# Performance work log

Measured on AMD Instinct MI355X. Metric: run time of the kernel, lower is better.

The kernel has to match this reference:

```python
import jax, jax.numpy as jnp
import numpy as np

B, L, E, H = 2, 2048, 1024, 16
D = E // H

def setup_inputs() -> dict:
    key = jax.random.key(0)
    ks = jax.random.split(key, 6)
    s = 1.0 / np.sqrt(E)
    return {
        "x": jax.random.normal(ks[0], (B, L, E), dtype=jnp.float32),
        "attention_mask": jnp.ones((B, L), dtype=jnp.float32),
        "Wq": jax.random.normal(ks[1], (E, E), dtype=jnp.float32) * s,
        "Wk": jax.random.normal(ks[2], (E, E), dtype=jnp.float32) * s,
        "Wv": jax.random.normal(ks[3], (E, E), dtype=jnp.float32) * s,
        "Wo": jax.random.normal(ks[4], (E, E), dtype=jnp.float32) * s,
        "bo": jnp.zeros((E,), dtype=jnp.float32),
    }

def reference(x, attention_mask, Wq, Wk, Wv, Wo, bo):
    b, l, e = x.shape
    h, d = H, D

    def proj(W):
        # (B,L,E) @ (E,E)^T -> (B,L,E) -> (B,H,L,D)
        return (x @ W.T).reshape(b, l, h, d).transpose(0, 2, 1, 3)

    q, k, v = proj(Wq), proj(Wk), proj(Wv)

    # multiplicative attention mask on q, k, v (mask shape (B,L) -> (B,1,L,1))
    m = attention_mask[:, None, :, None].astype(x.dtype)
    q, k, v = q * m, k * m, v * m

    scale = 1.0 / np.sqrt(d)
    scores = jnp.einsum('bhqd,bhkd->bhqk', q, k) * scale  # (B,H,L,L)
    causal = jnp.tril(jnp.ones((l, l), dtype=bool))
    scores = jnp.where(causal[None, None], scores, -jnp.inf)
    attn = jax.nn.softmax(scores, axis=-1)
    y = jnp.einsum('bhqk,bhkd->bhqd', attn, v)  # (B,H,L,D)
    y = y.transpose(0, 2, 1, 3).reshape(b, l, e)
    return y @ Wo.T + bo
```

## Files before the change

### kernel.cpp

```cpp
#include <hip/hip_runtime.h>
#include <cstdint>
#include <cstddef>
#include <math.h>

#define BB 2
#define LL 2048
#define EE 1024
#define HH 16
#define DD 64
#define MM (BB*LL)

typedef short short8 __attribute__((ext_vector_type(8)));
typedef float f32x4 __attribute__((ext_vector_type(4)));
typedef float f32x16 __attribute__((ext_vector_type(16)));

#define GPTR __attribute__((address_space(1)))
#define LPTR __attribute__((address_space(3)))

__device__ __forceinline__ unsigned short f32_bf16(float f) {
  union { float f; unsigned u; } c; c.f = f;
  c.u += 0x7fffu + ((c.u >> 16) & 1u);
  return (unsigned short)(c.u >> 16);
}

__device__ __forceinline__ unsigned pk_bf16(float lo, float hi) {
  unsigned r;
  asm("v_cvt_pk_bf16_f32 %0, %1, %2" : "=v"(r) : "v"(lo), "v"(hi));
  return r;
}
__device__ __forceinline__ void swap32(unsigned &a, unsigned &b) {
  asm("v_permlane32_swap_b32 %0, %1" : "+v"(a), "+v"(b));
}
__device__ __forceinline__ float xh_max(float v) {
  union { float f; unsigned u; } a, b;
  a.f = v;
  asm("v_mov_b32 %0, %1" : "=&v"(b.u) : "v"(a.u));
  asm("v_permlane32_swap_b32 %0, %1" : "+v"(a.u), "+v"(b.u));
  return fmaxf(a.f, b.f);
}
__device__ __forceinline__ float xh_sum(float v) {
  union { float f; unsigned u; } a, b;
  a.f = v;
  asm("v_mov_b32 %0, %1" : "=&v"(b.u) : "v"(a.u));
  asm("v_permlane32_swap_b32 %0, %1" : "+v"(a.u), "+v"(b.u));
  return a.f + b.f;
}
__device__ __forceinline__ f32x16 zero16() {
  f32x16 v;
  #pragma unroll
  for (int e = 0; e < 16; ++e) v[e] = 0.f;
  return v;
}

__global__ void cvt_all(const float* __restrict__ x,  const float* __restrict__ wq,
                        const float* __restrict__ wk, const float* __restrict__ wv,
                        const float* __restrict__ wo,
                        unsigned short* __restrict__ xb,  unsigned short* __restrict__ wqb,
                        unsigned short* __restrict__ wkb, unsigned short* __restrict__ wvb,
                        unsigned short* __restrict__ wob)
{
  int i = (blockIdx.x * 256 + threadIdx.x) * 4;
  if (i >= MM * EE + 4 * EE * EE) return;
  const float* s; unsigned short* d; int off;
  if (i < MM * EE) { s = x; d = xb; off = i; }
  else {
    int k = i - MM * EE;
    int w = k >> 20;
    off = k & (EE * EE - 1);
    s = (w == 0) ? wq : (w == 1) ? wk : (w == 2) ? wv : wo;
    d = (w == 0) ? wqb : (w == 1) ? wkb : (w == 2) ? wvb : wob;
  }
  float4 v = *(const float4*)(s + off);
  union { unsigned short s[4]; uint2 u; } o;
  o.s[0] = f32_bf16(v.x); o.s[1] = f32_bf16(v.y);
  o.s[2] = f32_bf16(v.z); o.s[3] = f32_bf16(v.w);
  *(uint2*)(d + off) = o.u;
}

template<int MODE>
__global__ __launch_bounds__(256, 2)
void gemm128(const unsigned short* __restrict__ A,
             const unsigned short* __restrict__ W0,
             const unsigned short* __restrict__ W1,
             const unsigned short* __restrict__ W2,
             const float* __restrict__ mask,
             const float* __restrict__ bias,
             unsigned short* __restrict__ O0,
             unsigned short* __restrict__ O1,
             unsigned short* __restrict__ O2,
             float* __restrict__ OF)
{
  constexpr int K = EE;
  const int tid = threadIdx.x;
  const int lane = tid & 63;
  const int wid = tid >> 6;
  const int g = lane >> 4, li = lane & 15;
  const int m0 = blockIdx.y * 128;
  const int n0 = blockIdx.x * 128;
  const int z = blockIdx.z;

  const unsigned short* Wp = W0;
  if (MODE == 0) Wp = (z == 0) ? W0 : ((z == 1) ? W1 : W2);

  __shared__ unsigned short As[128 * 64];
  __shared__ unsigned short Bs[128 * 64];

  f32x4 acc[4][4];
  f32x4 zero = {0.f, 0.f, 0.f, 0.f};
  #pragma unroll
  for (int i = 0; i < 4; ++i)
    #pragma unroll
    for (int j = 0; j < 4; ++j) acc[i][j] = zero;

  const int wm = (wid >> 1) * 64;
  const int wn = (wid & 1) * 64;

  for (int kt = 0; kt < K; kt += 64) {
    #pragma unroll
    for (int j = 0; j < 4; ++j) {
      int c = j * 256 + tid;
      int row = c >> 3;
      int lcol = ((c & 7) * 16) ^ ((row & 7) << 4);
      __builtin_amdgcn_global_load_lds(
        (const GPTR void*)((const char*)(A + (size_t)(m0 + row) * K + kt) + lcol),
        (LPTR void*)((char*)As + c * 16), 16, 0, 0);
      __builtin_amdgcn_global_load_lds(
        (const GPTR void*)((const char*)(Wp + (size_t)(n0 + row) * K + kt) + lcol),
        (LPTR void*)((char*)Bs + c * 16), 16, 0, 0);
    }
    __syncthreads();

    #pragma unroll
    for (int kk = 0; kk < 2; ++kk) {
      short8 a[4], b[4];
      const int colb = (kk * 32 + g * 8) * 2;
      #pragma unroll
      for (int i = 0; i < 4; ++i) {
        int ar = wm + i * 16 + li;
        a[i] = *(const short8*)((const char*)As + ar * 128 + (colb ^ ((ar & 7) << 4)));
        int br = wn + i * 16 + li;
        b[i] = *(const short8*)((const char*)Bs + br * 128 + (colb ^ ((br & 7) << 4)));
      }
      #pragma unroll
      for (int i = 0; i < 4; ++i)
        #pragma unroll
        for (int j = 0; j < 4; ++j)
          acc[i][j] = __builtin_amdgcn_mfma_f32_16x16x32_bf16(a[i], b[j], acc[i][j], 0, 0, 0);
    }
    __syncthreads();
  }

  if (MODE == 0) {
    if (z == 2) {
      #pragma unroll
      for (int i = 0; i < 4; ++i) {
        int mbase = m0 + wm + i * 16 + g * 4;
        int bb2 = mbase >> 11;
        int l0  = mbase & (LL - 1);
        float mk[4];
        #pragma unroll
        for (int r = 0; r < 4; ++r) mk[r] = mask[mbase + r];
        #pragma unroll
        for (int j = 0; j < 4; ++j) {
          int n = n0 + wn + j * 16 + li;
          int h2 = n >> 6, dd2 = n & 63;
          union { unsigned short s[4]; uint2 u; } o;
          #pragma unroll
          for (int r = 0; r < 4; ++r) o.s[r] = f32_bf16(acc[i][j][r] * mk[r]);
          size_t off = (size_t)(bb2 * HH + h2) * (LL * DD)
                     + (size_t)(l0 >> 5) * (DD * 32) + dd2 * 32 + (l0 & 31);
          *(uint2*)(O2 + off) = o.u;
        }
      }
    } else {
      unsigned short* Op = (z == 0) ? O0 : O1;
      const float sc = (z == 0) ? 0.125f * 1.44269504088896f : 1.0f;
      #pragma unroll
      for (int i = 0; i < 4; ++i) {
        #pragma unroll
        for (int r = 0; r < 4; ++r) {
          int m = m0 + wm + i * 16 + g * 4 + r;
          float mk = mask[m] * sc;
          int bb = m >> 11;
          int l  = m & (LL - 1);
          #pragma unroll
          for (int j = 0; j < 4; ++j) {
            int n = n0 + wn + j * 16 + li;
            int h = n >> 6, d = n & 63;
            size_t off = (((size_t)(bb * HH + h)) * LL + l) * DD + d;
            Op[off] = f32_bf16(acc[i][j][r] * mk);
          }
        }
      }
    }
  } else {
    #pragma unroll
    for (int i = 0; i < 4; ++i) {
      #pragma unroll
      for (int j = 0; j < 4; ++j) {
        int n = n0 + wn + j * 16 + li;
        float bv = bias[n];
        #pragma unroll
        for (int r = 0; r < 4; ++r) {
          int m = m0 + wm + i * 16 + g * 4 + r;
          OF[(size_t)m * EE + n] = acc[i][j][r] + bv;
        }
      }
    }
  }
}

__global__ __launch_bounds__(128)
void attn4(const unsigned short* __restrict__ Q,
           const unsigned short* __restrict__ K,
           const unsigned short* __restrict__ VT,
           unsigned short* __restrict__ Y)
{
  const int tid = threadIdx.x, lane = tid & 63, w = tid >> 6;
  const int l31 = lane & 31, hi = lane >> 5;

  const int id = blockIdx.x;
  const int lo = id & 7;
  const int r_ = id >> 3;
  const int bh = (r_ & 3) * 8 + lo;
  const int qt = 63 - (r_ >> 2);
  const int q0 = qt * 32;
  const int b = bh >> 4, h = bh & (HH - 1);
  const size_t kbase = (size_t)bh * LL * DD;

  const unsigned short* Kg  = K + kbase;
  const unsigned short* VTg = VT + kbase;

  const int qrow = q0 + l31;
  const int nt = qt + 1;

  short8 qf[4];
  {
    const unsigned short* Qr = Q + kbase + (size_t)qrow * DD + hi * 8;
    #pragma unroll
    for (int kc = 0; kc < 4; ++kc) qf[kc] = *(const short8*)(Qr + kc * 16);
  }

  f32x16 ot0 = zero16(), ot1 = zero16();
  float m = -INFINITY, lsum = 0.f;

  short8 kA[4], vA[4], kB[4], vB[4];

  auto loadtile = [&](short8 (&kk)[4], short8 (&vv)[4], int t2) {
    const int kv0 = t2 << 5;
    const unsigned short* Kp = Kg + ((size_t)(kv0 + l31) << 6) + hi * 8;
    #pragma unroll
    for (int kc = 0; kc < 4; ++kc) kk[kc] = *(const short8*)(Kp + kc * 16);
    const unsigned short* Vp = VTg + (size_t)(kv0 >> 5) * (DD * 32) + l31 * 32 + hi * 8;
    vv[0] = *(const short8*)(Vp);
    vv[1] = *(const short8*)(Vp + 16);
    vv[2] = *(const short8*)(Vp + 32 * 32);
    vv[3] = *(const short8*)(Vp + 32 * 32 + 16);
  };

  loadtile(kA, vA, w);

  auto body = [&](short8 (&ck)[4], short8 (&cv)[4],
                  short8 (&nk)[4], short8 (&nv)[4], int t) {
    if (t + 2 < nt) loadtile(nk, nv, t + 2);

    const int kv0 = t << 5;

    f32x16 s = zero16();
    __builtin_amdgcn_s_setprio(1);
    #pragma unroll
    for (int kc = 0; kc < 4; ++kc)
      s = __builtin_amdgcn_mfma_f32_32x32x16_bf16(ck[kc], qf[kc], s, 0, 0, 0);
    __builtin_amdgcn_s_setprio(0);

    if (t == nt - 1) {
      #pragma unroll
      for (int i = 0; i < 16; ++i) {
        int kvr = (i & 3) + 8 * (i >> 2) + 4 * hi;
        if (kvr > l31) s[i] = -INFINITY;
      }
    }

    float red[8];
    #pragma unroll
    for (int e = 0; e < 8; ++e) red[e] = fmaxf(s[e], s[e + 8]);
    #pragma unroll
    for (int st = 4; st >= 1; st >>= 1)
      #pragma unroll
      for (int e = 0; e < 4; ++e) if (e < st) red[e] = fmaxf(red[e], red[e + st]);
    float mv = xh_max(red[0]);

    if (!__all(mv <= m + 8.0f)) {
      float mnew = fmaxf(m, mv);
      float al = exp2f(m - mnew);
      m = mnew;
      lsum *= al;
      #pragma unroll
      for (int e = 0; e < 16; ++e) { ot0[e] *= al; ot1[e] *= al; }
    }

    float ra[8];
    #pragma unroll
    for (int e = 0; e < 16; ++e) s[e] = exp2f(s[e] - m);
    #pragma unroll
    for (int e = 0; e < 8; ++e) ra[e] = s[e] + s[e + 8];
    #pragma unroll
    for (int st = 4; st >= 1; st >>= 1)
      #pragma unroll
      for (int e = 0; e < 4; ++e) if (e < st) ra[e] += ra[e + st];
    lsum += xh_sum(ra[0]);

    auto mkfrag = [&](int base) -> short8 {
      unsigned a0 = pk_bf16(s[base + 0], s[base + 1]);
      unsigned a1 = pk_bf16(s[base + 2], s[base + 3]);
      unsigned b0 = pk_bf16(s[base + 4], s[base + 5]);
      unsigned b1 = pk_bf16(s[base + 6], s[base + 7]);
      swap32(a0, b0);
      swap32(a1, b1);
      union { unsigned u[4]; short8 s8; } f;
      f.u[0] = a0; f.u[1] = a1; f.u[2] = b0; f.u[3] = b1;
      return f.s8;
    };
    short8 pf0 = mkfrag(0), pf1 = mkfrag(8);

    __builtin_amdgcn_s_setprio(1);
    ot0 = __builtin_amdgcn_mfma_f32_32x32x16_bf16(cv[0], pf0, ot0, 0, 0, 0);
    ot0 = __builtin_amdgcn_mfma_f32_32x32x16_bf16(cv[1], pf1, ot0, 0, 0, 0);
    ot1 = __builtin_amdgcn_mfma_f32_32x32x16_bf16(cv[2], pf0, ot1, 0, 0, 0);
    ot1 = __builtin_amdgcn_mfma_f32_32x32x16_bf16(cv[3], pf1, ot1, 0, 0, 0);
    __builtin_amdgcn_s_setprio(0);
  };

  for (int t = w; t < nt; t += 4) {
    body(kA, vA, kB, vB, t);
    if (t + 2 < nt) body(kB, vB, kA, vA, t + 2);
  }

  __shared__ float mg[64][34];
  if (w == 1) {
    mg[lane][0] = m; mg[lane][1] = lsum;
    #pragma unroll
    for (int e = 0; e < 16; ++e) { mg[lane][2 + e] = ot0[e]; mg[lane][18 + e] = ot1[e]; }
  }
  __syncthreads();
  if (w == 0) {
    float m1 = mg[lane][0], l1 = mg[lane][1];
    float M = fmaxf(m, m1);
    float a0 = exp2f(m - M), a1 = exp2f(m1 - M);
    float Lt = lsum * a0 + l1 * a1;
    float inv = 1.0f / Lt;
    unsigned short* Yr = Y + ((size_t)b * LL + qrow) * EE + h * DD;
    #pragma unroll
    for (int rg = 0; rg < 4; ++rg) {
      union { unsigned short s[4]; uint2 u; } o0, o1;
      #pragma unroll
      for (int e = 0; e < 4; ++e) {
        int i = rg * 4 + e;
        o0.s[e] = f32_bf16((ot0[i] * a0 + mg[lane][2 + i]  * a1) * inv);
        o1.s[e] = f32_bf16((ot1[i] * a0 + mg[lane][18 + i] * a1) * inv);
      }
      *(uint2*)(Yr + rg * 8 + hi * 4) = o0.u;
      *(uint2*)(Yr + 32 + rg * 8 + hi * 4) = o1.u;
    }
  }
}

extern "C" void kernel_launch(void* const* d_in, const int* in_sizes, int n_in,
                              void* d_out, int out_size, void* d_ws, size_t ws_size,
                              hipStream_t stream) {
  const float* x    = (const float*)d_in[0];
  const float* mask = (const float*)d_in[1];
  const float* Wq   = (const float*)d_in[2];
  const float* Wk   = (const float*)d_in[3];
  const float* Wv   = (const float*)d_in[4];
  const float* Wo   = (const float*)d_in[5];
  const float* bo   = (const float*)d_in[6];
  float* out = (float*)d_out;

  char* ws = (char*)d_ws;
  unsigned short* xb  = (unsigned short*)(ws);
  unsigned short* wqb = (unsigned short*)(ws + ((size_t)8  << 20));
  unsigned short* wkb = (unsigned short*)(ws + ((size_t)10 << 20));
  unsigned short* wvb = (unsigned short*)(ws + ((size_t)12 << 20));
  unsigned short* wob = (unsigned short*)(ws + ((size_t)14 << 20));
  unsigned short* Qb  = (unsigned short*)(ws + ((size_t)16 << 20));
  unsigned short* Kb  = (unsigned short*)(ws + ((size_t)24 << 20));
  unsigned short* VTb = (unsigned short*)(ws + ((size_t)32 << 20));
  unsigned short* Yb  = (unsigned short*)(ws + ((size_t)40 << 20));

  cvt_all<<<8192, 256, 0, stream>>>(x, Wq, Wk, Wv, Wo, xb, wqb, wkb, wvb, wob);

  gemm128<0><<<dim3(EE / 128, MM / 128, 3), 256, 0, stream>>>(
      xb, wqb, wkb, wvb, mask, nullptr, Qb, Kb, VTb, nullptr);

  attn4<<<dim3(2048), 128, 0, stream>>>(Qb, Kb, VTb, Yb);

  gemm128<1><<<dim3(EE / 128, MM / 128, 1), 256, 0, stream>>>(
      Yb, wob, nullptr, nullptr, nullptr, bo, nullptr, nullptr, nullptr, out);
}
```

Measured before the change: 121.4 us.

## Pair high and low causal query tiles per block to share K/V loads

Each attention block now handles two query tiles, a late one (63-p) and an early one (p), instead of a single tile. Every block then does roughly the same causal work, and each K/V tile loaded for the long tile is reused for the short tile's QK and PV MFMAs. The grid is halved and the launch bounds gain a min-blocks hint of 2. The cost is roughly double the live registers (two Q fragment sets and two output accumulators) plus a larger LDS merge buffer, which risks spills or lower occupancy.

```diff
diff --git a/kernel.cpp b/kernel.cpp
--- a/kernel.cpp
+++ b/kernel.cpp
@@ -210,8 +210,8 @@
   }
 }
 
-__global__ __launch_bounds__(128)
-void attn4(const unsigned short* __restrict__ Q,
+__global__ __launch_bounds__(128, 2)
+void attn5(const unsigned short* __restrict__ Q,
            const unsigned short* __restrict__ K,
            const unsigned short* __restrict__ VT,
            unsigned short* __restrict__ Y)
@@ -223,26 +223,30 @@
   const int lo = id & 7;
   const int r_ = id >> 3;
   const int bh = (r_ & 3) * 8 + lo;
-  const int qt = 63 - (r_ >> 2);
-  const int q0 = qt * 32;
+  const int p  = r_ >> 2;
+  const int qth = 63 - p;
+  const int qtl = p;
   const int b = bh >> 4, h = bh & (HH - 1);
   const size_t kbase = (size_t)bh * LL * DD;
 
   const unsigned short* Kg  = K + kbase;
   const unsigned short* VTg = VT + kbase;
 
-  const int qrow = q0 + l31;
-  const int nt = qt + 1;
-
-  short8 qf[4];
+  const int qrh = qth * 32 + l31;
+  const int qrl = qtl * 32 + l31;
+
+  short8 qfh[4], qfl[4];
   {
-    const unsigned short* Qr = Q + kbase + (size_t)qrow * DD + hi * 8;
-    #pragma unroll
-    for (int kc = 0; kc < 4; ++kc) qf[kc] = *(const short8*)(Qr + kc * 16);
-  }
-
-  f32x16 ot0 = zero16(), ot1 = zero16();
-  float m = -INFINITY, lsum = 0.f;
+    const unsigned short* Qr = Q + kbase + (size_t)qrh * DD + hi * 8;
+    #pragma unroll
+    for (int kc = 0; kc < 4; ++kc) qfh[kc] = *(const short8*)(Qr + kc * 16);
+    const unsigned short* Qs = Q + kbase + (size_t)qrl * DD + hi * 8;
+    #pragma unroll
+    for (int kc = 0; kc < 4; ++kc) qfl[kc] = *(const short8*)(Qs + kc * 16);
+  }
+
+  f32x16 oh0 = zero16(), oh1 = zero16(), ol0 = zero16(), ol1 = zero16();
+  float mh = -INFINITY, lsh = 0.f, ml = -INFINITY, lsl = 0.f;
 
   short8 kA[4], vA[4], kB[4], vB[4];
 
@@ -260,27 +264,18 @@
 
   loadtile(kA, vA, w);
 
-  auto body = [&](short8 (&ck)[4], short8 (&cv)[4],
-                  short8 (&nk)[4], short8 (&nv)[4], int t) {
-    if (t + 2 < nt) loadtile(nk, nv, t + 2);
-
-    const int kv0 = t << 5;
-
+  auto qk = [&](const short8 (&ck)[4], const short8 (&qf)[4]) -> f32x16 {
     f32x16 s = zero16();
     __builtin_amdgcn_s_setprio(1);
     #pragma unroll
     for (int kc = 0; kc < 4; ++kc)
       s = __builtin_amdgcn_mfma_f32_32x32x16_bf16(ck[kc], qf[kc], s, 0, 0, 0);
     __builtin_amdgcn_s_setprio(0);
-
-    if (t == nt - 1) {
-      #pragma unroll
-      for (int i = 0; i < 16; ++i) {
-        int kvr = (i & 3) + 8 * (i >> 2) + 4 * hi;
-        if (kvr > l31) s[i] = -INFINITY;
-      }
-    }
-
+    return s;
+  };
+
+  auto process = [&](f32x16 s, const short8 (&cv)[4],
+                     float &mq, float &lq, f32x16 &o0, f32x16 &o1) {
     float red[8];
     #pragma unroll
     for (int e = 0; e < 8; ++e) red[e] = fmaxf(s[e], s[e + 8]);
@@ -290,25 +285,25 @@
       for (int e = 0; e < 4; ++e) if (e < st) red[e] = fmaxf(red[e], red[e + st]);
     float mv = xh_max(red[0]);
 
-    if (!__all(mv <= m + 8.0f)) {
-      float mnew = fmaxf(m, mv);
-      float al = exp2f(m - mnew);
-      m = mnew;
-      lsum *= al;
-      #pragma unroll
-      for (int e = 0; e < 16; ++e) { ot0[e] *= al; ot1[e] *= al; }
+    if (!__all(mv <= mq + 8.0f)) {
+      float mnew = fmaxf(mq, mv);
+      float al = exp2f(mq - mnew);
+      mq = mnew;
+      lq *= al;
+      #pragma unroll
+      for (int e = 0; e < 16; ++e) { o0[e] *= al; o1[e] *= al; }
     }
 
     float ra[8];
     #pragma unroll
-    for (int e = 0; e < 16; ++e) s[e] = exp2f(s[e] - m);
+    for (int e = 0; e < 16; ++e) s[e] = exp2f(s[e] - mq);
     #pragma unroll
     for (int e = 0; e < 8; ++e) ra[e] = s[e] + s[e + 8];
     #pragma unroll
     for (int st = 4; st >= 1; st >>= 1)
       #pragma unroll
       for (int e = 0; e < 4; ++e) if (e < st) ra[e] += ra[e + st];
-    lsum += xh_sum(ra[0]);
+    lq += xh_sum(ra[0]);
 
     auto mkfrag = [&](int base) -> short8 {
       unsigned a0 = pk_bf16(s[base + 0], s[base + 1]);
@@ -324,43 +319,83 @@
     short8 pf0 = mkfrag(0), pf1 = mkfrag(8);
 
     __builtin_amdgcn_s_setprio(1);
-    ot0 = __builtin_amdgcn_mfma_f32_32x32x16_bf16(cv[0], pf0, ot0, 0, 0, 0);
-    ot0 = __builtin_amdgcn_mfma_f32_32x32x16_bf16(cv[1], pf1, ot0, 0, 0, 0);
-    ot1 = __builtin_amdgcn_mfma_f32_32x32x16_bf16(cv[2], pf0, ot1, 0, 0, 0);
-    ot1 = __builtin_amdgcn_mfma_f32_32x32x16_bf16(cv[3], pf1, ot1, 0, 0, 0);
+    o0 = __builtin_amdgcn_mfma_f32_32x32x16_bf16(cv[0], pf0, o0, 0, 0, 0);
+    o0 = __builtin_amdgcn_mfma_f32_32x32x16_bf16(cv[1], pf1, o0, 0, 0, 0);
+    o1 = __builtin_amdgcn_mfma_f32_32x32x16_bf16(cv[2], pf0, o1, 0, 0, 0);
+    o1 = __builtin_amdgcn_mfma_f32_32x32x16_bf16(cv[3], pf1, o1, 0, 0, 0);
     __builtin_amdgcn_s_setprio(0);
   };
 
-  for (int t = w; t < nt; t += 4) {
+  auto body = [&](short8 (&ck)[4], short8 (&cv)[4],
+                  short8 (&nk)[4], short8 (&nv)[4], int t) {
+    if (t + 2 <= qth) loadtile(nk, nv, t + 2);
+
+    {
+      f32x16 s = qk(ck, qfh);
+      if (t == qth) {
+        #pragma unroll
+        for (int i = 0; i < 16; ++i) {
+          int kvr = (i & 3) + 8 * (i >> 2) + 4 * hi;
+          if (kvr > l31) s[i] = -INFINITY;
+        }
+      }
+      process(s, cv, mh, lsh, oh0, oh1);
+    }
+    if (t <= qtl) {
+      f32x16 s = qk(ck, qfl);
+      if (t == qtl) {
+        #pragma unroll
+        for (int i = 0; i < 16; ++i) {
+          int kvr = (i & 3) + 8 * (i >> 2) + 4 * hi;
+          if (kvr > l31) s[i] = -INFINITY;
+        }
+      }
+      process(s, cv, ml, lsl, ol0, ol1);
+    }
+  };
+
+  for (int t = w; t <= qth; t += 4) {
     body(kA, vA, kB, vB, t);
-    if (t + 2 < nt) body(kB, vB, kA, vA, t + 2);
-  }
-
-  __shared__ float mg[64][34];
+    if (t + 2 <= qth) body(kB, vB, kA, vA, t + 2);
+  }
+
+  __shared__ float mg[2][64][34];
   if (w == 1) {
-    mg[lane][0] = m; mg[lane][1] = lsum;
-    #pragma unroll
-    for (int e = 0; e < 16; ++e) { mg[lane][2 + e] = ot0[e]; mg[lane][18 + e] = ot1[e]; }
+    mg[0][lane][0] = mh; mg[0][lane][1] = lsh;
+    mg[1][lane][0] = ml; mg[1][lane][1] = lsl;
+    #pragma unroll
+    for (int e = 0; e < 16; ++e) {
+      mg[0][lane][2 + e] = oh0[e]; mg[0][lane][18 + e] = oh1[e];
+      mg[1][lane][2 + e] = ol0[e]; mg[1][lane][18 + e] = ol1[e];
+    }
   }
   __syncthreads();
   if (w == 0) {
-    float m1 = mg[lane][0], l1 = mg[lane][1];
-    float M = fmaxf(m, m1);
-    float a0 = exp2f(m - M), a1 = exp2f(m1 - M);
-    float Lt = lsum * a0 + l1 * a1;
-    float inv = 1.0f / Lt;
-    unsigned short* Yr = Y + ((size_t)b * LL + qrow) * EE + h * DD;
-    #pragma unroll
-    for (int rg = 0; rg < 4; ++rg) {
-      union { unsigned short s[4]; uint2 u; } o0, o1;
-      #pragma unroll
-      for (int e = 0; e < 4; ++e) {
-        int i = rg * 4 + e;
-        o0.s[e] = f32_bf16((ot0[i] * a0 + mg[lane][2 + i]  * a1) * inv);
-        o1.s[e] = f32_bf16((ot1[i] * a0 + mg[lane][18 + i] * a1) * inv);
-      }
-      *(uint2*)(Yr + rg * 8 + hi * 4) = o0.u;
-      *(uint2*)(Yr + 32 + rg * 8 + hi * 4) = o1.u;
+    #pragma unroll
+    for (int q = 0; q < 2; ++q) {
+      float mw = (q == 0) ? mh : ml;
+      float lw = (q == 0) ? lsh : lsl;
+      const f32x16& o0 = (q == 0) ? oh0 : ol0;
+      const f32x16& o1 = (q == 0) ? oh1 : ol1;
+      int qrow = (q == 0) ? qrh : qrl;
+      float m1 = mg[q][lane][0], l1 = mg[q][lane][1];
+      float M = fmaxf(mw, m1);
+      float a0 = exp2f(mw - M), a1 = exp2f(m1 - M);
+      float Lt = lw * a0 + l1 * a1;
+      float inv = 1.0f / Lt;
+      unsigned short* Yr = Y + ((size_t)b * LL + qrow) * EE + h * DD;
+      #pragma unroll
+      for (int rg = 0; rg < 4; ++rg) {
+        union { unsigned short s[4]; uint2 u; } u0, u1;
+        #pragma unroll
+        for (int e = 0; e < 4; ++e) {
+          int i = rg * 4 + e;
+          u0.s[e] = f32_bf16((o0[i] * a0 + mg[q][lane][2 + i]  * a1) * inv);
+          u1.s[e] = f32_bf16((o1[i] * a0 + mg[q][lane][18 + i] * a1) * inv);
+        }
+        *(uint2*)(Yr + rg * 8 + hi * 4) = u0.u;
+        *(uint2*)(Yr + 32 + rg * 8 + hi * 4) = u1.u;
+      }
     }
   }
 }
@@ -393,7 +428,7 @@
   gemm128<0><<<dim3(EE / 128, MM / 128, 3), 256, 0, stream>>>(
       xb, wqb, wkb, wvb, mask, nullptr, Qb, Kb, VTb, nullptr);
 
-  attn4<<<dim3(2048), 128, 0, stream>>>(Qb, Kb, VTb, Yb);
+  attn5<<<dim3(1024), 128, 0, stream>>>(Qb, Kb, VTb, Yb);
 
   gemm128<1><<<dim3(EE / 128, MM / 128, 1), 256, 0, stream>>>(
       Yb, wob, nullptr, nullptr, nullptr, bo, nullptr, nullptr, nullptr, out);
```

Result: faster. 111.1 us (-8.5%).
